# Performance work log

Hardware: AMD Instinct MI355X
Metric: run time of the kernel (lower is better)

Reference implementation:

```python
import jax, jax.numpy as jnp
import numpy as np
from jax import lax

B, N, F, H = 8, 2048, 256, 128
RATIO = 0.5
NUM_LAYERS = 2
K = int(N * RATIO) + 1  # num coarse nodes per layer


def setup_inputs() -> dict:
    key = jax.random.key(0)
    ks = jax.random.split(key, 8)
    x = jax.random.normal(ks[0], (B, N, F), dtype=jnp.float32)
    a = jax.random.uniform(ks[1], (B, N, N), dtype=jnp.float32)
    adj = (a < 0.005).astype(jnp.float32)
    adj = jnp.maximum(adj, adj.transpose(0, 2, 1))
    mask = jnp.ones((B, N), dtype=jnp.float32)
    W1 = jax.random.normal(ks[2], (F, H), dtype=jnp.float32) * (1.0 / np.sqrt(F))
    b1 = jnp.zeros((H,), dtype=jnp.float32)
    Watt = jax.random.normal(ks[3], (H, 1), dtype=jnp.float32) * (1.0 / np.sqrt(H))
    batt = jnp.zeros((1,), dtype=jnp.float32)
    W2 = jax.random.normal(ks[4], (H, F), dtype=jnp.float32) * (1.0 / np.sqrt(H))
    b2 = jnp.zeros((F,), dtype=jnp.float32)
    return {"x": x, "adj": adj, "mask": mask, "W1": W1, "b1": b1,
            "Watt": Watt, "batt": batt, "W2": W2, "b2": b2}


def dense_gcn(x, adj, W, b, mask):
    # PyG DenseGCNConv with add_loop=True: set diag to 1, sym-normalize, propagate
    n = adj.shape[-1]
    eye = jnp.eye(n, dtype=adj.dtype)
    a = adj * (1.0 - eye) + eye
    d = jnp.maximum(a.sum(-1), 1.0) ** -0.5            # [B,N]
    an = d[..., :, None] * a * d[..., None, :]
    out = jnp.einsum('bnm,bmh->bnh', an, x @ W) + b
    return out * mask[..., None]


def normalize_batch_adj(adj):
    n = adj.shape[-1]
    A = adj + jnp.eye(n, dtype=adj.dtype)
    d = jnp.maximum(A.sum(-1), 1.0) ** -0.5
    newA = d[..., :, None] * A * d[..., None, :]
    row_nonzero = (adj.sum(-1) > 0).astype(adj.dtype)  # zero out isolated-node rows
    return row_nonzero[..., None] * newA


def coarsen_block(x, adj, Watt, batt, k):
    norm_adj = normalize_batch_adj(adj)
    # attention GCN -> squared -> sigmoid
    alpha = jnp.einsum('bnm,bm->bn', norm_adj, (x @ Watt + batt).squeeze(-1))
    alpha = jax.nn.sigmoid(alpha ** 2)                 # [B,N]
    topv, topi = lax.top_k(alpha, k)
    cut = topv[:, -1]                                  # k-th largest value per graph
    cut_alpha = jax.nn.relu(alpha + 1e-7 - cut[:, None])
    S = norm_adj * cut_alpha[:, None, :]               # scale columns
    S = S / jnp.maximum(jnp.abs(S).sum(-1, keepdims=True), 1e-12)  # L1 row-normalize
    x2 = jnp.einsum('bnm,bnf->bmf', S, x)              # S^T x
    A2 = jnp.einsum('bnm,bnk,bkl->bml', S, adj, S)     # S^T A S
    A2 = jnp.floor(A2 * 1e4) / 1e4                     # 4-digit floor quantization
    return x2, A2, S, topi


def reference(x, adj, mask, W1, b1, Watt, batt, W2, b2):
    x1 = jax.nn.relu(dense_gcn(x, adj, W1, b1, mask))  # [B,N,H]
    coarse_x, new_adj = x1, adj
    for _ in range(NUM_LAYERS):
        coarse_x, new_adj, S, topi = coarsen_block(coarse_x, new_adj, Watt, batt, K)
    x2 = dense_gcn(coarse_x, new_adj, W2, b2, mask)    # [B,N,F]
    # JumpingKnowledge 'cat' of pooled readouts
    return jnp.concatenate([x1.mean(axis=1), x2.mean(axis=1)], axis=-1)  # [B,H+F]
```

## Files before the change

kernel.cpp:

```cpp
#include <hip/hip_runtime.h>
#include <math.h>

#define NN 2048
#define NB 8
#define FF 256
#define HH 128
#define KSEL 1025
#define NROWS (NB*NN)
#define MPAD 1152
#define MC (MPAD*NB)
#define LMAX 64
#define MI 6
#define RSTRIDE 2052
#define ZIDX 2048
#define LP 72

typedef unsigned short ushort_t;
typedef __attribute__((ext_vector_type(8))) short short8;
typedef __attribute__((ext_vector_type(4))) float f32x4;

__device__ inline ushort_t f2bf(float f) {
  unsigned u = __float_as_uint(f);
  unsigned r = (u + 0x7FFFu + ((u >> 16) & 1u)) >> 16;
  return (ushort_t)r;
}
__device__ inline float bf2f(ushort_t u) {
  unsigned x = ((unsigned)u) << 16;
  return __uint_as_float(x);
}

#define GLDS16(g, l) __builtin_amdgcn_global_load_lds( \
    (const __attribute__((address_space(1))) unsigned int*)(g), \
    (__attribute__((address_space(3))) unsigned int*)(l), 16, 0, 0)

__global__ __launch_bounds__(256) void rowstats_k(const float* __restrict__ A,
                                                  ushort_t* __restrict__ klist,
                                                  int* __restrict__ kcnt,
                                                  float* __restrict__ diag,
                                                  float* __restrict__ dgcn,
                                                  float* __restrict__ dnorm,
                                                  float* __restrict__ rz, int R) {
  int gw = (blockIdx.x * 256 + threadIdx.x) >> 6;
  int lane = threadIdx.x & 63;
  int b = gw / R, i = gw - b * R;
  const float4* row = (const float4*)(A + (long long)gw * R);
  int R4 = R >> 2;
  float s = 0.f;
  ushort_t* lst = klist ? (klist + (long long)gw * LMAX) : (ushort_t*)0;
  int base = 0;
  for (int j = lane; j < R4; j += 64) {
    float4 v = row[j];
    s += v.x + v.y + v.z + v.w;
    if (klist) {
      int c0 = (v.x != 0.f), c1 = (v.y != 0.f), c2 = (v.z != 0.f), c3 = (v.w != 0.f);
      int c = c0 + c1 + c2 + c3;
      int pref = c;
#pragma unroll
      for (int off = 1; off < 64; off <<= 1) {
        int t = __shfl_up(pref, off);
        if (lane >= off) pref += t;
      }
      int tot = __shfl(pref, 63);
      int p = base + pref - c;
      int col = j * 4;
      if (c0) { if (p < LMAX) lst[p] = (ushort_t)col;       p++; }
      if (c1) { if (p < LMAX) lst[p] = (ushort_t)(col + 1); p++; }
      if (c2) { if (p < LMAX) lst[p] = (ushort_t)(col + 2); p++; }
      if (c3) { if (p < LMAX) lst[p] = (ushort_t)(col + 3); p++; }
      base += tot;
    }
  }
  for (int off = 32; off > 0; off >>= 1) s += __shfl_down(s, off);
  if (lane == 0) {
    float dg = A[(long long)gw * R + i];
    diag[gw] = dg;
    dgcn[gw]  = rsqrtf(fmaxf(s - dg + 1.f, 1.f));
    dnorm[gw] = rsqrtf(fmaxf(s + 1.f, 1.f));
    rz[gw]    = s > 0.f ? 1.f : 0.f;
    if (kcnt) kcnt[gw] = base < LMAX ? base : LMAX;
  }
}

__global__ __launch_bounds__(256) void rowstatsw_k(const float* __restrict__ A,
                                                   const float* __restrict__ X,
                                                   const float* __restrict__ Watt,
                                                   const float* __restrict__ batt,
                                                   float* __restrict__ diag,
                                                   float* __restrict__ dgcn,
                                                   float* __restrict__ dnorm,
                                                   float* __restrict__ rz,
                                                   float* __restrict__ w, int R) {
  int gw = (blockIdx.x * 256 + threadIdx.x) >> 6;
  int lane = threadIdx.x & 63;
  int b = gw / R, i = gw - b * R;
  const float4* row = (const float4*)(A + (long long)gw * R);
  int R4 = R >> 2;
  float s = 0.f;
  for (int j = lane; j < R4; j += 64) {
    float4 v = row[j];
    s += v.x + v.y + v.z + v.w;
  }
  for (int off = 32; off > 0; off >>= 1) s += __shfl_xor(s, off);
  float dn = rsqrtf(fmaxf(s + 1.f, 1.f));
  const float* xr = X + (long long)gw * HH;
  float t = xr[lane] * Watt[lane] + xr[lane + 64] * Watt[lane + 64];
  for (int off = 32; off > 0; off >>= 1) t += __shfl_down(t, off);
  if (lane == 0) {
    float dg = A[(long long)gw * R + i];
    diag[gw] = dg;
    dgcn[gw]  = rsqrtf(fmaxf(s - dg + 1.f, 1.f));
    dnorm[gw] = dn;
    rz[gw]    = s > 0.f ? 1.f : 0.f;
    w[gw] = dn * (t + batt[0]);
  }
}

__global__ __launch_bounds__(256) void spmm1e_k(const ushort_t* __restrict__ klist,
                                                const int* __restrict__ kcnt,
                                                const float* __restrict__ dgcn,
                                                const float* __restrict__ diag,
                                                const float* __restrict__ b1,
                                                const float* __restrict__ mask,
                                                const float* __restrict__ Watt,
                                                const float* __restrict__ batt,
                                                const float* __restrict__ dnorm,
                                                const float* __restrict__ xw,
                                                float* __restrict__ xa,
                                                float* __restrict__ w) {
  int gw = (blockIdx.x * 256 + threadIdx.x) >> 6;
  int lane = threadIdx.x & 63;
  int b = gw >> 11;
  int cnt = kcnt[gw];
  const ushort_t* kl = klist + (long long)gw * LMAX;
  int myk = (lane < cnt) ? (int)kl[lane] : 0;
  float myd = dgcn[b * NN + myk];
  float s0 = 0.f, s1 = 0.f;
  for (int t = 0; t < cnt; t++) {
    int k = __shfl(myk, t);
    float d = __shfl(myd, t);
    const float* xr = xw + ((long long)b * NN + k) * HH;
    s0 += d * xr[lane];
    s1 += d * xr[lane + 64];
  }
  long long o = (long long)gw * HH;
  float d = dgcn[gw];
  float dgv = diag[gw];
  float mv = mask[gw];
  float xw0 = xw[o + lane], xw1v = xw[o + lane + 64];
  float t0 = d * (s0 + (1.f - dgv) * d * xw0) + b1[lane];
  float t1 = d * (s1 + (1.f - dgv) * d * xw1v) + b1[lane + 64];
  t0 *= mv; t1 *= mv;
  float x0 = fmaxf(t0, 0.f), x1 = fmaxf(t1, 0.f);
  xa[o + lane] = x0;
  xa[o + lane + 64] = x1;
  float t = x0 * Watt[lane] + x1 * Watt[lane + 64];
  for (int off = 32; off > 0; off >>= 1) t += __shfl_down(t, off);
  if (lane == 0) w[gw] = dnorm[gw] * (t + batt[0]);
}

__global__ __launch_bounds__(256) void spmm2_k(const ushort_t* __restrict__ klistC,
                                               const int* __restrict__ kcntC,
                                               const float* __restrict__ scalev,
                                               const float* __restrict__ cwk,
                                               const float* __restrict__ xa,
                                               float* __restrict__ x2c) {
  int gw = (blockIdx.x * 256 + threadIdx.x) >> 6;
  int lane = threadIdx.x & 63;
  int b = gw / MPAD;
  int cnt = kcntC[gw];
  const ushort_t* kl = klistC + (long long)gw * LP;
  int c64 = cnt < 64 ? cnt : 64;
  int myk = (lane < c64) ? (int)kl[lane] : 0;
  float myc = scalev[b * NN + myk];
  float s0 = 0.f, s1 = 0.f;
  for (int t = 0; t < c64; t++) {
    int k = __shfl(myk, t);
    float c = __shfl(myc, t);
    const float* xr = xa + ((long long)b * NN + k) * HH;
    s0 += c * xr[lane];
    s1 += c * xr[lane + 64];
  }
  if (cnt > 64) {
    int k = kl[64];
    float c = scalev[b * NN + k];
    const float* xr = xa + ((long long)b * NN + k) * HH;
    s0 += c * xr[lane];
    s1 += c * xr[lane + 64];
  }
  float cw = cwk[gw];
  long long o = (long long)gw * HH;
  x2c[o + lane] = cw * s0;
  x2c[o + lane + 64] = cw * s1;
}

__global__ __launch_bounds__(256) void alphaL_k(const ushort_t* __restrict__ klist,
                                                const int* __restrict__ kcnt,
                                                const float* __restrict__ w,
                                                const float* __restrict__ dnorm,
                                                const float* __restrict__ rz,
                                                float* __restrict__ alpha) {
  int gw = (blockIdx.x * 256 + threadIdx.x) >> 6;
  int lane = threadIdx.x & 63;
  int b = gw >> 11, i = gw & (NN - 1);
  int cnt = kcnt[gw];
  float s = 0.f;
  if (lane < cnt) s = w[(long long)b * NN + klist[(long long)gw * LMAX + lane]];
  for (int off = 32; off > 0; off >>= 1) s += __shfl_down(s, off);
  if (lane == 0) {
    float aa = rz[gw] * dnorm[gw] * (s + w[(long long)b * NN + i]);
    aa = aa * aa;
    alpha[(long long)b * NN + i] = 1.f / (1.f + expf(-aa));
  }
}

__global__ __launch_bounds__(256) void alpha_k(const float* __restrict__ A,
                                               const float* __restrict__ w,
                                               const float* __restrict__ dnorm,
                                               const float* __restrict__ rz,
                                               float* __restrict__ alpha, int R) {
  int gw = (blockIdx.x * 256 + threadIdx.x) >> 6;
  int lane = threadIdx.x & 63;
  int b = gw / R, i = gw - b * R;
  const float4* row = (const float4*)(A + (long long)gw * R);
  const float4* wb4 = (const float4*)(w + (long long)b * R);
  int R4 = R >> 2;
  float s = 0.f;
  for (int j = lane; j < R4; j += 64) {
    float4 a = row[j], ww = wb4[j];
    s += a.x * ww.x + a.y * ww.y + a.z * ww.z + a.w * ww.w;
  }
  for (int off = 32; off > 0; off >>= 1) s += __shfl_down(s, off);
  if (lane == 0) {
    float aa = rz[gw] * dnorm[gw] * (s + w[(long long)b * R + i]);
    aa = aa * aa;
    alpha[(long long)b * NN + i] = 1.f / (1.f + expf(-aa));
  }
}

__global__ __launch_bounds__(1024) void topkeep_k(const float* __restrict__ alpha,
                                                  const float* __restrict__ dnorm,
                                                  const float* __restrict__ rz,
                                                  float* __restrict__ colw,
                                                  int* __restrict__ keepidx) {
  __shared__ unsigned vals[NN];
  __shared__ int hist[256];
  __shared__ int wsum[32];
  __shared__ unsigned selp_s;
  __shared__ int selr_s;
  int b = blockIdx.x, t = threadIdx.x;
  vals[t] = __float_as_uint(alpha[b * NN + t]);
  vals[t + 1024] = __float_as_uint(alpha[b * NN + t + 1024]);
  if (t == 0) { selp_s = 0u; selr_s = KSEL; }
  __syncthreads();
  for (int shift = 24; shift >= 0; shift -= 8) {
    if (t < 256) hist[t] = 0;
    __syncthreads();
    unsigned pre = selp_s; int rank = selr_s;
    unsigned hm = (shift == 24) ? 0u : (0xFFFFFFFFu << (shift + 8));
    for (int e = t; e < NN; e += 1024) {
      unsigned v = vals[e];
      if ((v & hm) == (pre & hm)) atomicAdd(&hist[(v >> shift) & 255], 1);
    }
    __syncthreads();
    for (int off2 = 1; off2 < 256; off2 <<= 1) {
      int v = 0;
      if (t < 256 - off2) v = hist[t + off2];
      __syncthreads();
      if (t < 256 - off2) hist[t] += v;
      __syncthreads();
    }
    if (t < 256) {
      int cge = hist[t];
      int cgt = (t == 255) ? 0 : hist[t + 1];
      if (cge >= rank && cgt < rank) {
        selp_s = pre | ((unsigned)t << shift);
        selr_s = rank - cgt;
      }
    }
    __syncthreads();
  }
  float cu = __uint_as_float(selp_s);
  float a0 = __uint_as_float(vals[t]);
  float a1 = __uint_as_float(vals[t + 1024]);
  float c0 = dnorm[b * NN + t]        * fmaxf(a0 + 1e-7f - cu, 0.f);
  float c1 = dnorm[b * NN + t + 1024] * fmaxf(a1 + 1e-7f - cu, 0.f);
  colw[b * NN + t] = c0;
  colw[b * NN + t + 1024] = c1;
  int f0 = (c0 != 0.f && rz[b * NN + t]        != 0.f) ? 1 : 0;
  int f1 = (c1 != 0.f && rz[b * NN + t + 1024] != 0.f) ? 1 : 0;
  int lane = t & 63, wid = t >> 6;
  unsigned long long m0 = __ballot(f0);
  unsigned long long m1 = __ballot(f1);
  if (lane == 0) { wsum[wid] = __popcll(m0); wsum[16 + wid] = __popcll(m1); }
  __syncthreads();
  if (t == 0) { int run = 0; for (int i2 = 0; i2 < 32; i2++) { int v = wsum[i2]; wsum[i2] = run; run += v; } }
  __syncthreads();
  unsigned long long lm = (1ull << lane) - 1ull;
  int p0 = wsum[wid] + __popcll(m0 & lm);
  int p1 = wsum[16 + wid] + __popcll(m1 & lm);
  if (t < MPAD) keepidx[b * MPAD + t] = -1;
  if (t + 1024 < MPAD) keepidx[b * MPAD + t + 1024] = -1;
  __syncthreads();
  if (f0 && p0 < MPAD) keepidx[b * MPAD + p0] = t;
  if (f1 && p1 < MPAD) keepidx[b * MPAD + p1] = t + 1024;
}

__global__ __launch_bounds__(1024) void topcolw_k(const float* __restrict__ alpha,
                                                  const float* __restrict__ dnorm,
                                                  float* __restrict__ colw) {
  __shared__ unsigned vals[NN];
  __shared__ int hist[256];
  __shared__ unsigned selp_s;
  __shared__ int selr_s;
  int b = blockIdx.x, t = threadIdx.x;
  vals[t] = __float_as_uint(alpha[b * NN + t]);
  vals[t + 1024] = (t + 1024 >= MPAD) ? __float_as_uint(0.5f)
                                      : __float_as_uint(alpha[b * NN + t + 1024]);
  if (t == 0) { selp_s = 0u; selr_s = KSEL; }
  __syncthreads();
  for (int shift = 24; shift >= 0; shift -= 8) {
    if (t < 256) hist[t] = 0;
    __syncthreads();
    unsigned pre = selp_s; int rank = selr_s;
    unsigned hm = (shift == 24) ? 0u : (0xFFFFFFFFu << (shift + 8));
    for (int e = t; e < NN; e += 1024) {
      unsigned v = vals[e];
      if ((v & hm) == (pre & hm)) atomicAdd(&hist[(v >> shift) & 255], 1);
    }
    __syncthreads();
    for (int off2 = 1; off2 < 256; off2 <<= 1) {
      int v = 0;
      if (t < 256 - off2) v = hist[t + off2];
      __syncthreads();
      if (t < 256 - off2) hist[t] += v;
      __syncthreads();
    }
    if (t < 256) {
      int cge = hist[t];
      int cgt = (t == 255) ? 0 : hist[t + 1];
      if (cge >= rank && cgt < rank) {
        selp_s = pre | ((unsigned)t << shift);
        selr_s = rank - cgt;
      }
    }
    __syncthreads();
  }
  float cu = __uint_as_float(selp_s);
  for (int ii = t; ii < MPAD; ii += 1024) {
    float c = fmaxf(__uint_as_float(vals[ii]) + 1e-7f - cu, 0.f);
    colw[b * MPAD + ii] = dnorm[b * MPAD + ii] * c;
  }
}

__global__ __launch_bounds__(256) void scaleL_k(const ushort_t* __restrict__ klist,
                                                const int* __restrict__ kcnt,
                                                const float* __restrict__ colw,
                                                const float* __restrict__ dnorm,
                                                const float* __restrict__ rz,
                                                float* __restrict__ scale) {
  int gw = (blockIdx.x * 256 + threadIdx.x) >> 6;
  int lane = threadIdx.x & 63;
  int b = gw >> 11, i = gw & (NN - 1);
  int cnt = kcnt[gw];
  float s = 0.f;
  if (lane < cnt) s = colw[(long long)b * NN + klist[(long long)gw * LMAX + lane]];
  for (int off = 32; off > 0; off >>= 1) s += __shfl_down(s, off);
  if (lane == 0) {
    float rsum = rz[gw] * dnorm[gw] * (s + colw[(long long)b * NN + i]);
    scale[gw] = rz[gw] * dnorm[gw] / fmaxf(rsum, 1e-12f);
  }
}

__global__ __launch_bounds__(256) void scale_k(const float* __restrict__ A,
                                               const float* __restrict__ colw,
                                               const float* __restrict__ dnorm,
                                               const float* __restrict__ rz,
                                               float* __restrict__ scale, int R) {
  int gw = (blockIdx.x * 256 + threadIdx.x) >> 6;
  int lane = threadIdx.x & 63;
  int b = gw / R, i = gw - b * R;
  const float4* row = (const float4*)(A + (long long)gw * R);
  const float4* cw4 = (const float4*)(colw + (long long)b * R);
  int R4 = R >> 2;
  float s = 0.f;
  for (int j = lane; j < R4; j += 64) {
    float4 a = row[j], c = cw4[j];
    s += a.x * c.x + a.y * c.y + a.z * c.z + a.w * c.w;
  }
  for (int off = 32; off > 0; off >>= 1) s += __shfl_down(s, off);
  if (lane == 0) {
    float rsum = rz[gw] * dnorm[gw] * (s + colw[(long long)b * R + i]);
    scale[gw] = rz[gw] * dnorm[gw] / fmaxf(rsum, 1e-12f);
  }
}

__global__ __launch_bounds__(256) void packlist_k(const ushort_t* __restrict__ klist,
                                                  const int* __restrict__ kcnt,
                                                  const int* __restrict__ keepidx,
                                                  const float* __restrict__ colw,
                                                  ushort_t* __restrict__ klistC,
                                                  int* __restrict__ kcntC,
                                                  float* __restrict__ cwk) {
  int g = blockIdx.x * 256 + threadIdx.x;
  int b = g / MPAD;
  int rj = keepidx[g];
  ushort_t* dst = klistC + (long long)g * LP;
  int cnt = 0;
  if (rj >= 0) {
    long long gr = (long long)b * NN + rj;
    int c = kcnt[gr];
    const ushort_t* src = klist + gr * LMAX;
    for (int t = 0; t < c; t++) dst[t] = src[t];
    dst[c] = (ushort_t)rj;
    cnt = c + 1;
  }
  kcntC[g] = cnt;
  cwk[g] = (rj >= 0) ? colw[b * NN + rj] : 0.f;
  int pad = (cnt + 7) & ~7;
  for (int t = cnt; t < pad; t++) dst[t] = (ushort_t)ZIDX;
}

__global__ __launch_bounds__(256) void sparseA2f_k(const ushort_t* __restrict__ klist,
                                                   const int* __restrict__ kcnt,
                                                   const int* __restrict__ keepidx,
                                                   const float* __restrict__ scalev,
                                                   const ushort_t* __restrict__ klistC,
                                                   const int* __restrict__ kcntC,
                                                   const float* __restrict__ cwk,
                                                   float* __restrict__ A2cF,
                                                   ushort_t* __restrict__ A2cH,
                                                   ushort_t* __restrict__ A2cL) {
  __shared__ float Rs[3 * RSTRIDE * 2];
  int i0 = blockIdx.x * MI;
  int b = i0 / MPAD, im0 = i0 - b * MPAD;
  int tid = threadIdx.x;
  int wid = tid >> 6, lane = tid & 63;
  const float* sb = scalev + (long long)b * NN;

  float4 z4 = make_float4(0.f, 0.f, 0.f, 0.f);
  for (int n = tid * 4; n < 3 * RSTRIDE * 2; n += 1024) *(float4*)&Rs[n] = z4;
  __syncthreads();

  for (int rr = wid; rr < MI; rr += 4) {
    int r = keepidx[i0 + rr];
    if (r < 0) continue;
    int p = rr >> 1, q = rr & 1;
    float* plane = Rs + p * RSTRIDE * 2;
    long long gr = (long long)b * NN + r;
    int cr = kcnt[gr];
    int myk = (lane < cr) ? (int)klist[gr * LMAX + lane] : r;
    float mycoef = sb[myk];
    int mycnt = kcnt[(long long)b * NN + myk];
    for (int i = 0; i < cr; i++) {
      int k = __shfl(myk, i);
      float coef = __shfl(mycoef, i);
      int ck = __shfl(mycnt, i);
      if (lane < ck) {
        int n = (int)klist[((long long)b * NN + k) * LMAX + lane];
        plane[n * 2 + q] += coef;
      }
    }
    float coef = sb[r];
    if (lane < cr) plane[myk * 2 + q] += coef;
  }
  __syncthreads();

  for (int c = tid; c < NN; c += 256) {
    float sc = sb[c];
#pragma unroll
    for (int p = 0; p < 3; p++) {
      float2* e = (float2*)&Rs[(p * RSTRIDE + c) * 2];
      float2 v = *e; v.x *= sc; v.y *= sc; *e = v;
    }
  }
  __syncthreads();

  float cwi[MI];
#pragma unroll
  for (int r = 0; r < MI; r++) cwi[r] = cwk[i0 + r];
  long long ob = (long long)b * MPAD * MPAD + (long long)im0 * MPAD;
  for (int j = tid; j < MPAD; j += 256) {
    int cnt = kcntC[b * MPAD + j];
    const ushort_t* kl = klistC + (long long)(b * MPAD + j) * LP;
    float sx0 = 0.f, sy0 = 0.f, sx1 = 0.f, sy1 = 0.f, sx2 = 0.f, sy2 = 0.f;
    int rounds = (cnt + 7) >> 3;
    for (int t0 = 0; t0 < rounds; t0++) {
      uint4 kv = *(const uint4*)(kl + t0 * 8);
      const ushort_t* kp = (const ushort_t*)&kv;
#pragma unroll
      for (int t = 0; t < 8; t++) {
        int c = kp[t];
        float2 v0 = *(const float2*)&Rs[(0 * RSTRIDE + c) * 2];
        float2 v1 = *(const float2*)&Rs[(1 * RSTRIDE + c) * 2];
        float2 v2 = *(const float2*)&Rs[(2 * RSTRIDE + c) * 2];
        sx0 += v0.x; sy0 += v0.y;
        sx1 += v1.x; sy1 += v1.y;
        sx2 += v2.x; sy2 += v2.y;
      }
    }
    float sv[MI] = {sx0, sy0, sx1, sy1, sx2, sy2};
    float cwj = cwk[b * MPAD + j];
#pragma unroll
    for (int r = 0; r < MI; r++) {
      float vq = floorf(cwi[r] * cwj * sv[r] * 10000.f) / 10000.f;
      ushort_t h = f2bf(vq);
      long long o = ob + (long long)r * MPAD + j;
      A2cF[o] = vq;
      A2cH[o] = h;
      A2cL[o] = f2bf(vq - bf2f(h));
    }
  }
}

__global__ void writeS2c_k(const float* __restrict__ A2c, const float* __restrict__ scale,
                           const float* __restrict__ colw,
                           ushort_t* __restrict__ Sh, ushort_t* __restrict__ Sl) {
  int g = blockIdx.x * 256 + threadIdx.x;
  int bl = g / (MPAD / 4);
  int k = (g - bl * (MPAD / 4)) * 4;
  int b = bl / MPAD, l = bl - b * MPAD;
  long long o = (long long)bl * MPAD + k;
  float cw = colw[b * MPAD + l];
  float4 sc = *(const float4*)(scale + b * MPAD + k);
  float4 av = *(const float4*)(A2c + o);
  float v0 = sc.x * (av.x + (float)(k     == l)) * cw;
  float v1 = sc.y * (av.y + (float)(k + 1 == l)) * cw;
  float v2 = sc.z * (av.z + (float)(k + 2 == l)) * cw;
  float v3 = sc.w * (av.w + (float)(k + 3 == l)) * cw;
  ushort_t h0 = f2bf(v0), h1 = f2bf(v1), h2 = f2bf(v2), h3 = f2bf(v3);
  *(uint2*)&Sh[o] = make_uint2((unsigned)h0 | ((unsigned)h1 << 16),
                               (unsigned)h2 | ((unsigned)h3 << 16));
  ushort_t l0 = f2bf(v0 - bf2f(h0)), l1 = f2bf(v1 - bf2f(h1));
  ushort_t l2 = f2bf(v2 - bf2f(h2)), l3 = f2bf(v3 - bf2f(h3));
  *(uint2*)&Sl[o] = make_uint2((unsigned)l0 | ((unsigned)l1 << 16),
                               (unsigned)l2 | ((unsigned)l3 << 16));
}

template<int SA, int SB, int EPI, int BN>
__global__ __launch_bounds__(256) void mgemm_k(
    const ushort_t* __restrict__ Ah, const ushort_t* __restrict__ Al,
    const ushort_t* __restrict__ Bh, const ushort_t* __restrict__ Bl,
    float* __restrict__ Co, ushort_t* __restrict__ Toh, ushort_t* __restrict__ Tol,
    int M, int Ncol, int K, long long sA, long long sB, long long sC,
    int gx, int ks, long long sPart) {
  constexpr int NJ = BN / 32;
  __shared__ ushort_t Ahs[128 * 32];
  __shared__ ushort_t Bhs[BN * 32];
  __shared__ ushort_t Als[SA ? 128 * 32 : 64];
  __shared__ ushort_t Bls[SB ? BN * 32 : 64];

  int tid = threadIdx.x;
  int id = blockIdx.x;
  long long bz = id & 7;
  int rest = id >> 3;
  int kslice = rest % ks;
  int t0 = rest / ks;
  int tn = t0 % gx, tm = t0 / gx;
  int n0 = tn * BN, m0 = tm * 128;
  const ushort_t* Ahb = Ah + bz * sA;
  const ushort_t* Alb = SA ? (Al + bz * sA) : Ah;
  const ushort_t* Bhb = Bh + bz * sB;
  const ushort_t* Blb = SB ? (Bl + bz * sB) : Bh;

  int sr = tid >> 2;
  int sc = (tid & 3) * 8;
  int lane = tid & 63, w = tid >> 6;
  int wm = (w >> 1) * 64, wn = (w & 1) * (BN / 2);
  int fr = lane & 15;
  int fo = (lane >> 4) * 8;
  int q = lane >> 4;

  f32x4 acc[4][NJ];
  f32x4 zz = {0.f, 0.f, 0.f, 0.f};
#pragma unroll
  for (int i = 0; i < 4; i++)
#pragma unroll
    for (int j = 0; j < NJ; j++) acc[i][j] = zz;

  int Kpc = K / ks;
  int kbeg = kslice * Kpc;
  for (int k0 = kbeg; k0 < kbeg + Kpc; k0 += 32) {
    __syncthreads();
#pragma unroll
    for (int r = 0; r < 128; r += 64) {
      GLDS16(Ahb + (long long)(m0 + sr + r) * K + k0 + sc, &Ahs[(r + sr) * 32 + sc]);
      if constexpr (SA) {
        GLDS16(Alb + (long long)(m0 + sr + r) * K + k0 + sc, &Als[(r + sr) * 32 + sc]);
      }
    }
#pragma unroll
    for (int r = 0; r < BN; r += 64) {
      GLDS16(Bhb + (long long)(n0 + sr + r) * K + k0 + sc, &Bhs[(r + sr) * 32 + sc]);
      if constexpr (SB) {
        GLDS16(Blb + (long long)(n0 + sr + r) * K + k0 + sc, &Bls[(r + sr) * 32 + sc]);
      }
    }
    __syncthreads();

    short8 ah[4], al[4], bh[NJ], bl[NJ];
#pragma unroll
    for (int i = 0; i < 4; i++) {
      ah[i] = *(const short8*)&Ahs[(wm + i * 16 + fr) * 32 + fo];
      if constexpr (SA) al[i] = *(const short8*)&Als[(wm + i * 16 + fr) * 32 + fo];
    }
#pragma unroll
    for (int j = 0; j < NJ; j++) {
      bh[j] = *(const short8*)&Bhs[(wn + j * 16 + fr) * 32 + fo];
      if constexpr (SB) bl[j] = *(const short8*)&Bls[(wn + j * 16 + fr) * 32 + fo];
    }
#pragma unroll
    for (int i = 0; i < 4; i++)
#pragma unroll
      for (int j = 0; j < NJ; j++) {
        acc[i][j] = __builtin_amdgcn_mfma_f32_16x16x32_bf16(ah[i], bh[j], acc[i][j], 0, 0, 0);
        if constexpr (SB)
          acc[i][j] = __builtin_amdgcn_mfma_f32_16x16x32_bf16(ah[i], bl[j], acc[i][j], 0, 0, 0);
        if constexpr (SA)
          acc[i][j] = __builtin_amdgcn_mfma_f32_16x16x32_bf16(al[i], bh[j], acc[i][j], 0, 0, 0);
      }
  }

#pragma unroll
  for (int i = 0; i < 4; i++)
#pragma unroll
    for (int j = 0; j < NJ; j++)
#pragma unroll
      for (int r = 0; r < 4; r++) {
        float v = acc[i][j][r];
        int row = m0 + wm + i * 16 + q * 4 + r;
        int col = n0 + wn + j * 16 + fr;
        long long idx = bz * sC + (long long)row * Ncol + col;
        if constexpr (EPI == 0) {
          Co[kslice * sPart + idx] = v;
        } else if constexpr (EPI == 1) {
          ushort_t h = f2bf(v);
          Toh[idx] = h;
          Tol[idx] = f2bf(v - bf2f(h));
        } else {
          Co[idx] = floorf(v * 10000.f) / 10000.f;
        }
      }
}

__global__ __launch_bounds__(256) void wfin_k(const float* __restrict__ A3,
                                              const float* __restrict__ dgcn,
                                              const float* __restrict__ diag,
                                              float* __restrict__ wv) {
  int gw = (blockIdx.x * 256 + threadIdx.x) >> 6;
  int lane = threadIdx.x & 63;
  int b = gw / MPAD;
  const float4* row = (const float4*)(A3 + (long long)gw * MPAD);
  const float4* d4 = (const float4*)(dgcn + (long long)b * MPAD);
  float s = 0.f;
  for (int j = lane; j < MPAD / 4; j += 64) {
    float4 a = row[j], d = d4[j];
    s += a.x * d.x + a.y * d.y + a.z * d.z + a.w * d.w;
  }
  for (int off = 32; off > 0; off >>= 1) s += __shfl_down(s, off);
  if (lane == 0) {
    float dl = dgcn[gw];
    wv[gw] = dl * (s - dl * diag[gw] + dl);
  }
}

__global__ __launch_bounds__(256) void zfin_k(const float* __restrict__ A2c,
                                              const float* __restrict__ scalev,
                                              const float* __restrict__ colwv,
                                              const float* __restrict__ wv,
                                              float* __restrict__ zv) {
  int gw = (blockIdx.x * 256 + threadIdx.x) >> 6;
  int lane = threadIdx.x & 63;
  int b = gw / MPAD;
  const float4* row = (const float4*)(A2c + (long long)gw * MPAD);
  const float4* c4 = (const float4*)(colwv + (long long)b * MPAD);
  const float4* w4 = (const float4*)(wv + (long long)b * MPAD);
  float s = 0.f;
  for (int j = lane; j < MPAD / 4; j += 64) {
    float4 a = row[j], c = c4[j], w = w4[j];
    s += a.x * c.x * w.x + a.y * c.y * w.y + a.z * c.z * w.z + a.w * c.w * w.w;
  }
  for (int off = 32; off > 0; off >>= 1) s += __shfl_down(s, off);
  if (lane == 0) {
    zv[gw] = scalev[gw] * (s + colwv[gw] * wv[gw]);
  }
}

__global__ void zx_k(const float* __restrict__ zv, const float* __restrict__ x2c,
                     float* __restrict__ part) {
  int b = blockIdx.y, c = blockIdx.x, h = threadIdx.x;
  const float* p = x2c + ((long long)(b * MPAD + c * 128)) * HH + h;
  const float* zp = zv + b * MPAD + c * 128;
  float s = 0.f;
  for (int r = 0; r < 128; r++) s += zp[r] * p[(long long)r * HH];
  part[(b * 9 + c) * HH + h] = s;
}

__global__ __launch_bounds__(256) void fout2_k(const float* __restrict__ part,
                                               const float* __restrict__ W2,
                                               const float* __restrict__ b2,
                                               float* __restrict__ out) {
  __shared__ float wx3[HH];
  int b = blockIdx.x, f = threadIdx.x;
  if (f < HH) {
    float s = 0.f;
    for (int c = 0; c < 9; c++) s += part[(b * 9 + c) * HH + f];
    wx3[f] = s;
  }
  __syncthreads();
  float s = 0.f;
  for (int h = 0; h < HH; h++) s += wx3[h] * W2[h * FF + f];
  out[b * (HH + FF) + HH + f] = b2[f] + s * (1.f / NN);
}

__global__ void pmean_k(const float* __restrict__ X, float* __restrict__ part,
                        int Nn, int Fd, int rpc) {
  int b = blockIdx.y, c = blockIdx.x, f = threadIdx.x;
  const float* p = X + ((long long)b * Nn + (long long)c * rpc) * Fd + f;
  float s = 0.f;
  for (int r = 0; r < rpc; r++) s += p[(long long)r * Fd];
  part[((long long)b * gridDim.x + c) * Fd + f] = s;
}

__global__ void fmean_k(const float* __restrict__ part, int nch, int Fd, float corr,
                        const float* __restrict__ bias, float* __restrict__ out, int outoff) {
  int b = blockIdx.x, f = threadIdx.x;
  float s = 0.f;
  for (int c = 0; c < nch; c++) s += part[((long long)b * nch + c) * Fd + f];
  float cv = bias ? corr * bias[f] : 0.f;
  out[b * (HH + FF) + outoff + f] = s * (1.f / NN) + cv;
}

__global__ __launch_bounds__(256) void gemm_k(const float* __restrict__ A, const float* __restrict__ B,
                                              float* __restrict__ C,
                                              const float* __restrict__ rsc,
                                              ushort_t* __restrict__ Th, ushort_t* __restrict__ Tl,
                                              int M, int Nw, int Kk, int Nn,
                                              long long sA, long long sB, long long sC) {
  __shared__ float As[16][128];
  __shared__ float Bs[16][128];
  int tid = threadIdx.x;
  int n0 = blockIdx.x * 128, m0 = blockIdx.y * 128;
  int bz = blockIdx.z;
  const float* Ab = A + (long long)bz * sA;
  const float* Bb = B + (long long)bz * sB;
  float* Cb = C + (long long)bz * sC;
  float acc[8][8];
#pragma unroll
  for (int i = 0; i < 8; i++)
#pragma unroll
    for (int j = 0; j < 8; j++) acc[i][j] = 0.f;
  int tx = tid & 15, ty = tid >> 4;

  for (int k0 = 0; k0 < Kk; k0 += 16) {
    {
      int r = tid >> 2, c = (tid & 3) << 2;
#pragma unroll
      for (int rr = 0; rr < 2; rr++) {
        int rrow = r + rr * 64;
        float4 v = *(const float4*)(Ab + (long long)(m0 + rrow) * Kk + k0 + c);
        As[c + 0][rrow] = v.x; As[c + 1][rrow] = v.y;
        As[c + 2][rrow] = v.z; As[c + 3][rrow] = v.w;
      }
    }
    {
      int kk = tid >> 5, cc = (tid & 31) << 2;
#pragma unroll
      for (int k2 = 0; k2 < 2; k2++) {
        float4 v = *(const float4*)(Bb + (long long)(k0 + kk + k2 * 8) * Nw + n0 + cc);
        *(float4*)&Bs[kk + k2 * 8][cc] = v;
      }
    }
    __syncthreads();
#pragma unroll
    for (int kk = 0; kk < 16; kk++) {
      float a[8], bb[8];
      *(float4*)&a[0]  = *(float4*)&As[kk][ty * 8];
      *(float4*)&a[4]  = *(float4*)&As[kk][ty * 8 + 4];
      *(float4*)&bb[0] = *(float4*)&Bs[kk][tx * 8];
      *(float4*)&bb[4] = *(float4*)&Bs[kk][tx * 8 + 4];
#pragma unroll
      for (int i = 0; i < 8; i++)
#pragma unroll
        for (int j = 0; j < 8; j++) acc[i][j] += a[i] * bb[j];
    }
    __syncthreads();
  }
#pragma unroll
  for (int i = 0; i < 8; i++) {
    float* cp = Cb + (long long)(m0 + ty * 8 + i) * Nw + n0 + tx * 8;
    *(float4*)cp = *(float4*)&acc[i][0];
    *(float4*)(cp + 4) = *(float4*)&acc[i][4];
  }
  if (Th) {
#pragma unroll
    for (int j = 0; j < 8; j++) {
      int col = n0 + tx * 8 + j;
      ushort_t hs[8], ls[8];
#pragma unroll
      for (int i = 0; i < 8; i++) {
        int r2 = m0 + ty * 8 + i;
        float v = rsc[(long long)bz * Nn + r2] * acc[i][j];
        hs[i] = f2bf(v);
        ls[i] = f2bf(v - bf2f(hs[i]));
      }
      long long o = ((long long)bz * Nw + col) * Nn + m0 + ty * 8;
      *(uint4*)&Th[o] = *(uint4*)hs;
      *(uint4*)&Tl[o] = *(uint4*)ls;
    }
  }
}

extern "C" void kernel_launch(void* const* d_in, const int* in_sizes, int n_in,
                              void* d_out, int out_size, void* d_ws, size_t ws_size,
                              hipStream_t stream) {
  const float* x    = (const float*)d_in[0];
  const float* adj  = (const float*)d_in[1];
  const float* mask = (const float*)d_in[2];
  const float* W1   = (const float*)d_in[3];
  const float* b1   = (const float*)d_in[4];
  const float* Watt = (const float*)d_in[5];
  const float* batt = (const float*)d_in[6];
  const float* W2   = (const float*)d_in[7];
  const float* b2   = (const float*)d_in[8];
  float* out = (float*)d_out;

  const long long CSTR = (long long)MPAD * NN;
  const long long CTOT = (long long)NB * CSTR;
  const long long M2   = (long long)MPAD * MPAD;
  const long long M2T  = (long long)NB * M2;
  const long long NH   = (long long)NROWS * HH;
  const long long MH   = (long long)MC * HH;

  float* ws = (float*)d_ws;
  long long off = 0;
  ushort_t* S2cH = (ushort_t*)(ws + off); off += M2T;
  float* A2CR = ws + off; off += M2T * 2;
  float* TcF  = ws + off; off += CTOT;
  float* A3F  = ws + off; off += CTOT / 2;
  float* xa   = ws + off; off += NH;
  float* x2c  = ws + off; off += MH;
  float* x3c  = ws + off; off += MH;
  float* diag   = ws + off; off += NROWS;
  float* dgcn   = ws + off; off += NROWS;
  float* dnorm  = ws + off; off += NROWS;
  float* rz     = ws + off; off += NROWS;
  float* wv     = ws + off; off += NROWS;
  float* alphav = ws + off; off += (long long)NB * NN;
  float* colwv  = ws + off; off += NROWS;
  float* scalev = ws + off; off += NROWS;
  off += NROWS / 2;
  off += NROWS / 2;
  int* keepidx  = (int*)(ws + off); off += NB * MPAD;
  float* cwk    = ws + off; off += MC;
  float* partm  = ws + off; off += NB * 16 * FF;

  ushort_t* S2cL = S2cH + M2T;
  float* A2cF = A2CR;
  ushort_t* A2cH = (ushort_t*)(A2CR + M2T);
  ushort_t* A2cL = A2cH + M2T;

  ushort_t* klist = (ushort_t*)x3c;
  int* kcnt = (int*)(x3c + (long long)NROWS * (LMAX / 2));
  ushort_t* klistC = (ushort_t*)(x3c + (long long)NROWS * (LMAX / 2) + NROWS);
  int* kcntC = (int*)(x3c + (long long)NROWS * (LMAX / 2) + NROWS + (long long)MC * LP / 2);

  float* u1 = TcF;
  ushort_t* Tc2H = (ushort_t*)TcF;
  ushort_t* Tc2L = Tc2H + M2T;

  rowstats_k<<<NROWS / 4, 256, 0, stream>>>(adj, klist, kcnt, diag, dgcn, dnorm, rz, NN);
  gemm_k<<<dim3(1, NN / 128, NB), 256, 0, stream>>>(
      x, W1, u1, 0, 0, 0, NN, HH, FF, NN,
      (long long)NN * FF, 0, (long long)NN * HH);
  spmm1e_k<<<NROWS / 4, 256, 0, stream>>>(klist, kcnt, dgcn, diag, b1, mask,
                                          Watt, batt, dnorm, u1, xa, wv);
  pmean_k<<<dim3(16, NB), HH, 0, stream>>>(xa, partm, NN, HH, 128);
  fmean_k<<<NB, HH, 0, stream>>>(partm, 16, HH, 0.f, 0, out, 0);

  alphaL_k<<<NROWS / 4, 256, 0, stream>>>(klist, kcnt, wv, dnorm, rz, alphav);
  topkeep_k<<<NB, 1024, 0, stream>>>(alphav, dnorm, rz, colwv, keepidx);
  scaleL_k<<<NROWS / 4, 256, 0, stream>>>(klist, kcnt, colwv, dnorm, rz, scalev);
  packlist_k<<<MC / 256, 256, 0, stream>>>(klist, kcnt, keepidx, colwv, klistC, kcntC, cwk);
  sparseA2f_k<<<MC / MI, 256, 0, stream>>>(klist, kcnt, keepidx, scalev,
                                           klistC, kcntC, cwk, A2cF, A2cH, A2cL);
  spmm2_k<<<MC / 4, 256, 0, stream>>>(klistC, kcntC, scalev, cwk, xa, x2c);

  rowstatsw_k<<<MC / 4, 256, 0, stream>>>(A2cF, x2c, Watt, batt, diag, dgcn, dnorm, rz, wv, MPAD);
  alpha_k<<<MC / 4, 256, 0, stream>>>(A2cF, wv, dnorm, rz, alphav, MPAD);
  topcolw_k<<<NB, 1024, 0, stream>>>(alphav, dnorm, colwv);
  scale_k<<<MC / 4, 256, 0, stream>>>(A2cF, colwv, dnorm, rz, scalev, MPAD);
  writeS2c_k<<<(int)(M2T / 4 / 256), 256, 0, stream>>>(A2cF, scalev, colwv, S2cH, S2cL);
  mgemm_k<1, 1, 1, 64><<<(MPAD / 128) * (MPAD / 64) * NB, 256, 0, stream>>>(
      S2cH, S2cL, A2cH, A2cL, 0, Tc2H, Tc2L,
      MPAD, MPAD, MPAD, M2, M2, M2, MPAD / 64, 1, 0);
  mgemm_k<1, 1, 6, 64><<<(MPAD / 128) * (MPAD / 64) * NB, 256, 0, stream>>>(
      S2cH, S2cL, Tc2H, Tc2L, A3F, 0, 0,
      MPAD, MPAD, MPAD, M2, M2, M2, MPAD / 64, 1, 0);

  rowstats_k<<<MC / 4, 256, 0, stream>>>(A3F, 0, 0, diag, dgcn, dnorm, rz, MPAD);
  wfin_k<<<MC / 4, 256, 0, stream>>>(A3F, dgcn, diag, wv);
  zfin_k<<<MC / 4, 256, 0, stream>>>(A2cF, scalev, colwv, wv, alphav );
  zx_k<<<dim3(9, NB), HH, 0, stream>>>(alphav, x2c, partm);
  fout2_k<<<NB, FF, 0, stream>>>(partm, W2, b2, out);
}
```

Baseline: 703.2 us.

## Fuse final row-sum and diagonal extraction into GEMM epilogue; swizzle SpMM block order

```diff
diff --git a/kernel.cpp b/kernel.cpp
--- a/kernel.cpp
+++ b/kernel.cpp
@@ -85,14 +85,12 @@
                                                    const float* __restrict__ X,
                                                    const float* __restrict__ Watt,
                                                    const float* __restrict__ batt,
-                                                   float* __restrict__ diag,
-                                                   float* __restrict__ dgcn,
                                                    float* __restrict__ dnorm,
                                                    float* __restrict__ rz,
                                                    float* __restrict__ w, int R) {
   int gw = (blockIdx.x * 256 + threadIdx.x) >> 6;
   int lane = threadIdx.x & 63;
-  int b = gw / R, i = gw - b * R;
+  int b = gw / R;
   const float4* row = (const float4*)(A + (long long)gw * R);
   int R4 = R >> 2;
   float s = 0.f;
@@ -106,9 +104,6 @@
   float t = xr[lane] * Watt[lane] + xr[lane + 64] * Watt[lane + 64];
   for (int off = 32; off > 0; off >>= 1) t += __shfl_down(t, off);
   if (lane == 0) {
-    float dg = A[(long long)gw * R + i];
-    diag[gw] = dg;
-    dgcn[gw]  = rsqrtf(fmaxf(s - dg + 1.f, 1.f));
     dnorm[gw] = dn;
     rz[gw]    = s > 0.f ? 1.f : 0.f;
     w[gw] = dn * (t + batt[0]);
@@ -127,7 +122,9 @@
                                                 const float* __restrict__ xw,
                                                 float* __restrict__ xa,
                                                 float* __restrict__ w) {
-  int gw = (blockIdx.x * 256 + threadIdx.x) >> 6;
+  int bid = blockIdx.x;
+  int sw = (bid & 7) * ((int)gridDim.x >> 3) + (bid >> 3);
+  int gw = (sw * 256 + threadIdx.x) >> 6;
   int lane = threadIdx.x & 63;
   int b = gw >> 11;
   int cnt = kcnt[gw];
@@ -164,7 +161,9 @@
                                                const float* __restrict__ cwk,
                                                const float* __restrict__ xa,
                                                float* __restrict__ x2c) {
-  int gw = (blockIdx.x * 256 + threadIdx.x) >> 6;
+  int bid = blockIdx.x;
+  int sw = (bid & 7) * ((int)gridDim.x >> 3) + (bid >> 3);
+  int gw = (sw * 256 + threadIdx.x) >> 6;
   int lane = threadIdx.x & 63;
   int b = gw / MPAD;
   int cnt = kcntC[gw];
@@ -420,6 +419,10 @@
   for (int t = cnt; t < pad; t++) dst[t] = (ushort_t)ZIDX;
 }
 
+__global__ void zero_k(float* __restrict__ p) {
+  p[blockIdx.x * 256 + threadIdx.x] = 0.f;
+}
+
 __global__ __launch_bounds__(256) void sparseA2f_k(const ushort_t* __restrict__ klist,
                                                    const int* __restrict__ kcnt,
                                                    const int* __restrict__ keepidx,
@@ -541,6 +544,7 @@
     const ushort_t* __restrict__ Ah, const ushort_t* __restrict__ Al,
     const ushort_t* __restrict__ Bh, const ushort_t* __restrict__ Bl,
     float* __restrict__ Co, ushort_t* __restrict__ Toh, ushort_t* __restrict__ Tol,
+    float* __restrict__ rs, float* __restrict__ dgv,
     int M, int Ncol, int K, long long sA, long long sB, long long sC,
     int gx, int ks, long long sPart) {
   constexpr int NJ = BN / 32;
@@ -620,26 +624,52 @@
       }
   }
 
-#pragma unroll
-  for (int i = 0; i < 4; i++)
-#pragma unroll
-    for (int j = 0; j < NJ; j++)
+  if constexpr (EPI == 6) {
+#pragma unroll
+    for (int i = 0; i < 4; i++)
 #pragma unroll
       for (int r = 0; r < 4; r++) {
-        float v = acc[i][j][r];
         int row = m0 + wm + i * 16 + q * 4 + r;
-        int col = n0 + wn + j * 16 + fr;
-        long long idx = bz * sC + (long long)row * Ncol + col;
-        if constexpr (EPI == 0) {
-          Co[kslice * sPart + idx] = v;
-        } else if constexpr (EPI == 1) {
-          ushort_t h = f2bf(v);
-          Toh[idx] = h;
-          Tol[idx] = f2bf(v - bf2f(h));
-        } else {
-          Co[idx] = floorf(v * 10000.f) / 10000.f;
+        long long rb = bz * sC + (long long)row * Ncol;
+        float rp = 0.f;
+#pragma unroll
+        for (int j = 0; j < NJ; j++) {
+          int col = n0 + wn + j * 16 + fr;
+          float vq = floorf(acc[i][j][r] * 10000.f) / 10000.f;
+          Co[rb + col] = vq;
+          rp += vq;
+          if (col == row) dgv[bz * MPAD + row] = vq;
         }
-      }
+#pragma unroll
+        for (int o2 = 8; o2 > 0; o2 >>= 1) rp += __shfl_down(rp, o2, 16);
+        if (fr == 0) atomicAdd(&rs[bz * MPAD + row], rp);
+      }
+  } else {
+#pragma unroll
+    for (int i = 0; i < 4; i++)
+#pragma unroll
+      for (int j = 0; j < NJ; j++)
+#pragma unroll
+        for (int r = 0; r < 4; r++) {
+          float v = acc[i][j][r];
+          int row = m0 + wm + i * 16 + q * 4 + r;
+          int col = n0 + wn + j * 16 + fr;
+          long long idx = bz * sC + (long long)row * Ncol + col;
+          if constexpr (EPI == 0) {
+            Co[kslice * sPart + idx] = v;
+          } else {
+            ushort_t h = f2bf(v);
+            Toh[idx] = h;
+            Tol[idx] = f2bf(v - bf2f(h));
+          }
+        }
+  }
+}
+
+__global__ void dstat_k(const float* __restrict__ rs, const float* __restrict__ dgv,
+                        float* __restrict__ dgcn) {
+  int g = blockIdx.x * 256 + threadIdx.x;
+  dgcn[g] = rsqrtf(fmaxf(rs[g] - dgv[g] + 1.f, 1.f));
 }
 
 __global__ __launch_bounds__(256) void wfin_k(const float* __restrict__ A3,
@@ -732,9 +762,7 @@
 
 __global__ __launch_bounds__(256) void gemm_k(const float* __restrict__ A, const float* __restrict__ B,
                                               float* __restrict__ C,
-                                              const float* __restrict__ rsc,
-                                              ushort_t* __restrict__ Th, ushort_t* __restrict__ Tl,
-                                              int M, int Nw, int Kk, int Nn,
+                                              int M, int Nw, int Kk,
                                               long long sA, long long sB, long long sC) {
   __shared__ float As[16][128];
   __shared__ float Bs[16][128];
@@ -790,23 +818,6 @@
     float* cp = Cb + (long long)(m0 + ty * 8 + i) * Nw + n0 + tx * 8;
     *(float4*)cp = *(float4*)&acc[i][0];
     *(float4*)(cp + 4) = *(float4*)&acc[i][4];
-  }
-  if (Th) {
-#pragma unroll
-    for (int j = 0; j < 8; j++) {
-      int col = n0 + tx * 8 + j;
-      ushort_t hs[8], ls[8];
-#pragma unroll
-      for (int i = 0; i < 8; i++) {
-        int r2 = m0 + ty * 8 + i;
-        float v = rsc[(long long)bz * Nn + r2] * acc[i][j];
-        hs[i] = f2bf(v);
-        ls[i] = f2bf(v - bf2f(hs[i]));
-      }
-      long long o = ((long long)bz * Nw + col) * Nn + m0 + ty * 8;
-      *(uint4*)&Th[o] = *(uint4*)hs;
-      *(uint4*)&Tl[o] = *(uint4*)ls;
-    }
   }
 }
 
@@ -868,9 +879,11 @@
   ushort_t* Tc2H = (ushort_t*)TcF;
   ushort_t* Tc2L = Tc2H + M2T;
 
+  float* rsum = alphav;
+
   rowstats_k<<<NROWS / 4, 256, 0, stream>>>(adj, klist, kcnt, diag, dgcn, dnorm, rz, NN);
   gemm_k<<<dim3(1, NN / 128, NB), 256, 0, stream>>>(
-      x, W1, u1, 0, 0, 0, NN, HH, FF, NN,
+      x, W1, u1, NN, HH, FF,
       (long long)NN * FF, 0, (long long)NN * HH);
   spmm1e_k<<<NROWS / 4, 256, 0, stream>>>(klist, kcnt, dgcn, diag, b1, mask,
                                           Watt, batt, dnorm, u1, xa, wv);
@@ -885,19 +898,20 @@
                                            klistC, kcntC, cwk, A2cF, A2cH, A2cL);
   spmm2_k<<<MC / 4, 256, 0, stream>>>(klistC, kcntC, scalev, cwk, xa, x2c);
 
-  rowstatsw_k<<<MC / 4, 256, 0, stream>>>(A2cF, x2c, Watt, batt, diag, dgcn, dnorm, rz, wv, MPAD);
+  rowstatsw_k<<<MC / 4, 256, 0, stream>>>(A2cF, x2c, Watt, batt, dnorm, rz, wv, MPAD);
   alpha_k<<<MC / 4, 256, 0, stream>>>(A2cF, wv, dnorm, rz, alphav, MPAD);
   topcolw_k<<<NB, 1024, 0, stream>>>(alphav, dnorm, colwv);
   scale_k<<<MC / 4, 256, 0, stream>>>(A2cF, colwv, dnorm, rz, scalev, MPAD);
   writeS2c_k<<<(int)(M2T / 4 / 256), 256, 0, stream>>>(A2cF, scalev, colwv, S2cH, S2cL);
   mgemm_k<1, 1, 1, 64><<<(MPAD / 128) * (MPAD / 64) * NB, 256, 0, stream>>>(
-      S2cH, S2cL, A2cH, A2cL, 0, Tc2H, Tc2L,
+      S2cH, S2cL, A2cH, A2cL, 0, Tc2H, Tc2L, 0, 0,
       MPAD, MPAD, MPAD, M2, M2, M2, MPAD / 64, 1, 0);
+  zero_k<<<MC / 256, 256, 0, stream>>>(rsum);
   mgemm_k<1, 1, 6, 64><<<(MPAD / 128) * (MPAD / 64) * NB, 256, 0, stream>>>(
-      S2cH, S2cL, Tc2H, Tc2L, A3F, 0, 0,
+      S2cH, S2cL, Tc2H, Tc2L, A3F, 0, 0, rsum, diag,
       MPAD, MPAD, MPAD, M2, M2, M2, MPAD / 64, 1, 0);
 
-  rowstats_k<<<MC / 4, 256, 0, stream>>>(A3F, 0, 0, diag, dgcn, dnorm, rz, MPAD);
+  dstat_k<<<MC / 256, 256, 0, stream>>>(rsum, diag, dgcn);
   wfin_k<<<MC / 4, 256, 0, stream>>>(A3F, dgcn, diag, wv);
   zfin_k<<<MC / 4, 256, 0, stream>>>(A2cF, scalev, colwv, wv, alphav );
   zx_k<<<dim3(9, NB), HH, 0, stream>>>(alphav, x2c, partm);
```

Result: no change. 694.2 us (-1.3%).
